# Performance work log

Measured on AMD Instinct MI355X. Metric: run time of the kernel, lower is better.

The kernel has to match this reference:

```python
import jax, jax.numpy as jnp
import numpy as np

T = 464
H = 256  # 256 * network_scale**2 with network_scale=1


def setup_inputs() -> dict:
    key = jax.random.key(0)
    ks = jax.random.split(key, 8)
    B = 64
    feature_encoded = jax.random.normal(ks[0], (B, T, H), dtype=jnp.float32)
    memory_state = jax.random.normal(ks[1], (B, H), dtype=jnp.float32) * 0.1
    carry_state = jax.random.normal(ks[2], (B, H), dtype=jnp.float32) * 0.1
    # LSTM params: kernel [H, 4H], recurrent kernel [H, 4H], bias [4H]; gate order i,f,c,o (Keras)
    # small init scale keeps the relu-activated recurrence numerically stable over 464 steps
    W = jax.random.normal(ks[3], (H, 4 * H), dtype=jnp.float32) * 0.02
    U = jax.random.normal(ks[4], (H, 4 * H), dtype=jnp.float32) * 0.02
    b = jnp.zeros((4 * H,), dtype=jnp.float32)
    # trailing dense: Flatten([B, T, H]) -> Dense(H, relu)
    Wd = jax.random.normal(ks[5], (T * H, H), dtype=jnp.float32) * (1.0 / np.sqrt(T * H))
    bd = jnp.zeros((H,), dtype=jnp.float32)
    return {"feature_encoded": feature_encoded, "memory_state": memory_state,
            "carry_state": carry_state, "W": W, "U": U, "b": b, "Wd": Wd, "bd": bd}


def _lstm_relu(x, h0, c0, W, U, b):
    # Keras LSTM with activation='relu', recurrent_activation='sigmoid'.
    def step(carry, x_t):
        h, c = carry
        z = x_t @ W + h @ U + b           # [B, 4H]
        zi, zf, zg, zo = jnp.split(z, 4, axis=-1)
        i = jax.nn.sigmoid(zi)
        f = jax.nn.sigmoid(zf)
        c = f * c + i * jax.nn.relu(zg)
        o = jax.nn.sigmoid(zo)
        h = o * jax.nn.relu(c)
        return (h, c), h

    xs = jnp.swapaxes(x, 0, 1)            # [T, B, H]
    (hT, cT), ys = jax.lax.scan(step, (h0, c0), xs)
    return jnp.swapaxes(ys, 0, 1), hT, cT  # [B, T, H], [B, H], [B, H]


def reference(feature_encoded, memory_state, carry_state, W, U, b, Wd, bd):
    B = feature_encoded.shape[0]
    x = feature_encoded.reshape(B, T, H)
    seq, hT, cT = _lstm_relu(x, memory_state, carry_state, W, U, b)
    flat = seq.reshape(B, T * H)
    core_output = jax.nn.relu(flat @ Wd + bd)  # [B, H]
    return core_output, hT, cT
```

## Files before the change

### kernel.cpp

```cpp
#include <hip/hip_runtime.h>

#define TT  464
#define HH  256
#define BB  64
#define NWG 64

using bf16x8 = __attribute__((ext_vector_type(8))) short;
using f32x4  = __attribute__((ext_vector_type(4))) float;

__device__ __forceinline__ unsigned short f2bf(float x) {
  union { float f; unsigned u; } v; v.f = x;
  unsigned r = v.u + 0x7fffu + ((v.u >> 16) & 1u);
  return (unsigned short)(r >> 16);
}

__device__ __forceinline__ void wait_flags(int* flags, int base, int target) {
  const int ln  = threadIdx.x & 63;
  int* p = &flags[base + (ln & 31)];
  for (;;) {
    int f = __hip_atomic_load(p, __ATOMIC_RELAXED, __HIP_MEMORY_SCOPE_AGENT);
    if (__all(f >= target)) break;
    __builtin_amdgcn_s_sleep(1);
  }
  asm volatile("" ::: "memory");
}

__global__ __launch_bounds__(256) void lstm_kernel(
    const float* __restrict__ x,
    const float* __restrict__ h0,
    const float* __restrict__ c0,
    const float* __restrict__ W,
    const float* __restrict__ U,
    const float* __restrict__ bias,
    unsigned int* __restrict__ h_bufs,
    unsigned short* __restrict__ seq,
    float* __restrict__ out,
    int* __restrict__ flags)
{
  const int tid = threadIdx.x;
  const int wg  = blockIdx.x;
  const int bgi = wg >> 5;
  const int fgi = wg & 31;
  const int wv  = tid >> 6;
  const int ln  = tid & 63;
  const int mt  = wv >> 1;
  const int nt  = wv & 1;
  const int l15 = ln & 15;
  const int q   = ln >> 4;

  __shared__ unsigned short Bt[32][520];
  __shared__ unsigned short x_lds[32][264];
  __shared__ float          z_lds[32][36];

  for (int it = 0; it < 64; ++it) {
    int i  = it * 256 + tid;
    int k  = i >> 5;
    int n  = i & 31;
    int gc = (n >> 3) * 256 + fgi * 8 + (n & 7);
    float wval = (k < 256) ? W[(size_t)k * 1024 + gc] : U[(size_t)(k - 256) * 1024 + gc];
    Bt[n][k] = f2bf(wval);
  }

  const int r_own = tid >> 3;
  const int j_own = tid & 7;
  const int brow  = bgi * 32 + r_own;
  const int col   = fgi * 8 + j_own;
  float c = c0[brow * HH + col];
  float h = h0[brow * HH + col];
  const float b_i = bias[        col];
  const float b_f = bias[  HH  + col];
  const float b_g = bias[2*HH  + col];
  const float b_o = bias[3*HH  + col];

  {
    unsigned short hb16 = f2bf(h);
    unsigned other = (unsigned)(unsigned short)__shfl_xor((int)hb16, 1);
    if (!(tid & 1)) {
      unsigned hpk = (unsigned)hb16 | (other << 16);
      __hip_atomic_store(&h_bufs[brow * 128 + (col >> 1)], hpk,
                         __ATOMIC_RELAXED, __HIP_MEMORY_SCOPE_AGENT);
    }
  }

  const int xc0  = j_own * 32;
  float4 xr[8];
  {
    const float4* p = (const float4*)(x + ((size_t)brow * TT + 0) * HH + xc0);
#pragma unroll
    for (int i = 0; i < 8; ++i) xr[i] = p[i];
  }

  __builtin_amdgcn_s_waitcnt(0);
  __syncthreads();
  if (tid == 0)
    __hip_atomic_store(&flags[wg], 1, __ATOMIC_RELAXED, __HIP_MEMORY_SCOPE_AGENT);

  for (int t = 0; t < TT; ++t) {
    const int pr  = t & 1;
    const int pwb = pr ^ 1;

    {
      unsigned px[16];
#pragma unroll
      for (int i = 0; i < 8; ++i) {
        px[2*i]   = (unsigned)f2bf(xr[i].x) | ((unsigned)f2bf(xr[i].y) << 16);
        px[2*i+1] = (unsigned)f2bf(xr[i].z) | ((unsigned)f2bf(xr[i].w) << 16);
      }
#pragma unroll
      for (int s = 0; s < 4; ++s) {
        uint4 v = make_uint4(px[4*s], px[4*s+1], px[4*s+2], px[4*s+3]);
        *(uint4*)&x_lds[r_own][xc0 + s * 8] = v;
      }
    }
    {
      const int tn = (t + 1 < TT) ? (t + 1) : (TT - 1);
      const float4* p = (const float4*)(x + ((size_t)brow * TT + tn) * HH + xc0);
#pragma unroll
      for (int i = 0; i < 8; ++i) xr[i] = p[i];
    }

    __syncthreads();

    f32x4 acc = {0.f, 0.f, 0.f, 0.f};
#pragma unroll
    for (int kk = 0; kk < 8; ++kk) {
      bf16x8 afr = *(const bf16x8*)&x_lds[mt * 16 + l15][kk * 32 + q * 8];
      bf16x8 bfr = *(const bf16x8*)&Bt[nt * 16 + l15][kk * 32 + q * 8];
      acc = __builtin_amdgcn_mfma_f32_16x16x32_bf16(afr, bfr, acc, 0, 0, 0);
    }

    wait_flags(flags, bgi * 32, t + 1);

    bf16x8 hf[8];
    {
      const unsigned long long* hb = (const unsigned long long*)h_bufs
          + (size_t)pr * (BB * HH / 4) + (bgi * 32 + mt * 16 + l15) * (HH / 4) + q * 2;
#pragma unroll
      for (int kk = 0; kk < 8; ++kk) {
        union { unsigned long long u[2]; bf16x8 v; } tmp;
        tmp.u[0] = __hip_atomic_load(hb + kk * 8 + 0, __ATOMIC_RELAXED, __HIP_MEMORY_SCOPE_AGENT);
        tmp.u[1] = __hip_atomic_load(hb + kk * 8 + 1, __ATOMIC_RELAXED, __HIP_MEMORY_SCOPE_AGENT);
        hf[kk] = tmp.v;
      }
    }
#pragma unroll
    for (int kk = 0; kk < 8; ++kk) {
      bf16x8 bfr = *(const bf16x8*)&Bt[nt * 16 + l15][256 + kk * 32 + q * 8];
      acc = __builtin_amdgcn_mfma_f32_16x16x32_bf16(hf[kk], bfr, acc, 0, 0, 0);
    }
#pragma unroll
    for (int reg = 0; reg < 4; ++reg)
      z_lds[mt * 16 + q * 4 + reg][nt * 16 + l15] = acc[reg];

    __syncthreads();

    float zi = z_lds[r_own][      j_own] + b_i;
    float zf = z_lds[r_own][ 8 + j_own] + b_f;
    float zg = z_lds[r_own][16 + j_own] + b_g;
    float zo = z_lds[r_own][24 + j_own] + b_o;
    float gi = 1.f / (1.f + __expf(-zi));
    float gf = 1.f / (1.f + __expf(-zf));
    float go = 1.f / (1.f + __expf(-zo));
    float gg = fmaxf(zg, 0.f);
    c = gf * c + gi * gg;
    h = go * fmaxf(c, 0.f);
    unsigned short hb16 = f2bf(h);
    seq[((size_t)brow * TT + t) * HH + col] = hb16;

    {
      unsigned other = (unsigned)(unsigned short)__shfl_xor((int)hb16, 1);
      if (!(tid & 1)) {
        unsigned hpk = (unsigned)hb16 | (other << 16);
        __hip_atomic_store(&h_bufs[pwb * (BB * 128) + brow * 128 + (col >> 1)], hpk,
                           __ATOMIC_RELAXED, __HIP_MEMORY_SCOPE_AGENT);
      }
    }
    __builtin_amdgcn_s_waitcnt(0);
    __syncthreads();
    if (tid == 0)
      __hip_atomic_store(&flags[wg], t + 2, __ATOMIC_RELAXED, __HIP_MEMORY_SCOPE_AGENT);
  }

  out[16384 + brow * HH + col] = h;
  out[32768 + brow * HH + col] = c;
}

#define DP_PA 264
#define DP_PW 258
__global__ __launch_bounds__(256) void dense_partial(
    const unsigned short* __restrict__ seq,
    const float* __restrict__ Wd,
    float* __restrict__ part)
{
  __shared__ __align__(16) char smem[64 * DP_PA * 2];
  unsigned short* a_lds = (unsigned short*)smem;
  float*          Wf    = (float*)smem;

  const int kb  = blockIdx.x;
  const int tid = threadIdx.x;
  const int wv  = tid >> 6;
  const int ln  = tid & 63;
  const int l15 = ln & 15;
  const int q   = ln >> 4;

  f32x4 acc[16];
#pragma unroll
  for (int i = 0; i < 16; ++i) acc[i] = (f32x4){0.f, 0.f, 0.f, 0.f};

  for (int half = 0; half < 2; ++half) {
    const int t = kb + half * 232;
    __syncthreads();
#pragma unroll
    for (int it = 0; it < 8; ++it) {
      int cidx = it * 256 + tid;
      int row  = cidx >> 5;
      int off  = (cidx & 31) * 8;
      *(bf16x8*)&a_lds[row * DP_PA + off] =
          *(const bf16x8*)(seq + ((size_t)row * TT + t) * HH + off);
    }
    __syncthreads();
    bf16x8 af[8];
#pragma unroll
    for (int kk = 0; kk < 8; ++kk)
      af[kk] = *(const bf16x8*)&a_lds[(wv * 16 + l15) * DP_PA + kk * 32 + q * 8];

    for (int ck = 0; ck < 8; ++ck) {
      __syncthreads();
#pragma unroll
      for (int it = 0; it < 8; ++it) {
        int idx = it * 256 + tid;
        int r   = idx >> 6;
        int c4  = (idx & 63) * 4;
        float4 v = *(const float4*)(Wd + ((size_t)(t * 256 + ck * 32 + r)) * HH + c4);
        *(float2*)&Wf[r * DP_PW + c4]     = make_float2(v.x, v.y);
        *(float2*)&Wf[r * DP_PW + c4 + 2] = make_float2(v.z, v.w);
      }
      __syncthreads();
#pragma unroll
      for (int nt2 = 0; nt2 < 16; ++nt2) {
        const int n = nt2 * 16 + l15;
        bf16x8 bfr;
#pragma unroll
        for (int j = 0; j < 8; ++j)
          bfr[j] = (short)f2bf(Wf[(q * 8 + j) * DP_PW + n]);
        acc[nt2] = __builtin_amdgcn_mfma_f32_16x16x32_bf16(af[ck], bfr, acc[nt2], 0, 0, 0);
      }
    }
  }

  float* pb = part + (size_t)kb * (BB * HH);
#pragma unroll
  for (int nt2 = 0; nt2 < 16; ++nt2)
#pragma unroll
    for (int reg = 0; reg < 4; ++reg)
      pb[(wv * 16 + q * 4 + reg) * HH + nt2 * 16 + l15] = acc[nt2][reg];
}

__global__ __launch_bounds__(256) void dense_reduce(
    const float* __restrict__ part,
    const float* __restrict__ bd,
    float* __restrict__ out)
{
  const int o = blockIdx.x * 256 + threadIdx.x;
  float s0 = 0.f, s1 = 0.f, s2 = 0.f, s3 = 0.f;
  for (int kb = 0; kb < 232; kb += 4) {
    s0 += part[(size_t)(kb    ) * 16384 + o];
    s1 += part[(size_t)(kb + 1) * 16384 + o];
    s2 += part[(size_t)(kb + 2) * 16384 + o];
    s3 += part[(size_t)(kb + 3) * 16384 + o];
  }
  float s = (s0 + s1) + (s2 + s3) + bd[o & 255];
  out[o] = fmaxf(s, 0.f);
}

extern "C" void kernel_launch(void* const* d_in, const int* in_sizes, int n_in,
                              void* d_out, int out_size, void* d_ws, size_t ws_size,
                              hipStream_t stream) {
  const float* x  = (const float*)d_in[0];
  const float* h0 = (const float*)d_in[1];
  const float* c0 = (const float*)d_in[2];
  const float* W  = (const float*)d_in[3];
  const float* U  = (const float*)d_in[4];
  const float* bv = (const float*)d_in[5];
  const float* Wd = (const float*)d_in[6];
  const float* bd = (const float*)d_in[7];
  float* out = (float*)d_out;

  char* w = (char*)d_ws;
  int* flags = (int*)w;
  unsigned int*   h_bufs = (unsigned int*)(w + 256);
  unsigned short* seq    = (unsigned short*)(w + 256 + 2 * BB * HH * 2);
  float*          part   = (float*)(w + 256 + 2 * BB * HH * 2 + (size_t)BB * TT * HH * 2);

  hipMemsetAsync(d_ws, 0, 256, stream);
  lstm_kernel<<<NWG, 256, 0, stream>>>(x, h0, c0, W, U, bv, h_bufs, seq, out, flags);
  dense_partial<<<232, 256, 0, stream>>>(seq, Wd, part);
  dense_reduce<<<64, 256, 0, stream>>>(part, bd, out);
}
```

Before: 2.334 ms.

## Replace flag barrier with step-tagged h values and keep LSTM weights in registers

```diff
diff --git a/kernel.cpp b/kernel.cpp
--- a/kernel.cpp
+++ b/kernel.cpp
@@ -7,6 +7,8 @@
 
 using bf16x8 = __attribute__((ext_vector_type(8))) short;
 using f32x4  = __attribute__((ext_vector_type(4))) float;
+typedef unsigned long long u64;
+typedef unsigned int u32;
 
 __device__ __forceinline__ unsigned short f2bf(float x) {
   union { float f; unsigned u; } v; v.f = x;
@@ -14,28 +16,16 @@
   return (unsigned short)(r >> 16);
 }
 
-__device__ __forceinline__ void wait_flags(int* flags, int base, int target) {
-  const int ln  = threadIdx.x & 63;
-  int* p = &flags[base + (ln & 31)];
-  for (;;) {
-    int f = __hip_atomic_load(p, __ATOMIC_RELAXED, __HIP_MEMORY_SCOPE_AGENT);
-    if (__all(f >= target)) break;
-    __builtin_amdgcn_s_sleep(1);
-  }
-  asm volatile("" ::: "memory");
-}
-
-__global__ __launch_bounds__(256) void lstm_kernel(
+__global__ __launch_bounds__(256, 1) void lstm_kernel(
     const float* __restrict__ x,
     const float* __restrict__ h0,
     const float* __restrict__ c0,
     const float* __restrict__ W,
     const float* __restrict__ U,
     const float* __restrict__ bias,
-    unsigned int* __restrict__ h_bufs,
+    u32* __restrict__ h_bufs,
     unsigned short* __restrict__ seq,
-    float* __restrict__ out,
-    int* __restrict__ flags)
+    float* __restrict__ out)
 {
   const int tid = threadIdx.x;
   const int wg  = blockIdx.x;
@@ -48,17 +38,19 @@
   const int l15 = ln & 15;
   const int q   = ln >> 4;
 
-  __shared__ unsigned short Bt[32][520];
-  __shared__ unsigned short x_lds[32][264];
-  __shared__ float          z_lds[32][36];
-
-  for (int it = 0; it < 64; ++it) {
-    int i  = it * 256 + tid;
-    int k  = i >> 5;
-    int n  = i & 31;
-    int gc = (n >> 3) * 256 + fgi * 8 + (n & 7);
-    float wval = (k < 256) ? W[(size_t)k * 1024 + gc] : U[(size_t)(k - 256) * 1024 + gc];
-    Bt[n][k] = f2bf(wval);
+  __shared__ float z_lds[2][32][36];
+
+  const int n  = nt * 16 + l15;
+  const int gc = (n >> 3) * 256 + fgi * 8 + (n & 7);
+  bf16x8 Bw[8], Bu[8];
+#pragma unroll
+  for (int kk = 0; kk < 8; ++kk) {
+#pragma unroll
+    for (int j = 0; j < 8; ++j) {
+      const int k = kk * 32 + q * 8 + j;
+      Bw[kk][j] = (short)f2bf(W[(size_t)k * 1024 + gc]);
+      Bu[kk][j] = (short)f2bf(U[(size_t)k * 1024 + gc]);
+    }
   }
 
   const int r_own = tid >> 3;
@@ -72,113 +64,98 @@
   const float b_g = bias[2*HH  + col];
   const float b_o = bias[3*HH  + col];
 
-  {
-    unsigned short hb16 = f2bf(h);
-    unsigned other = (unsigned)(unsigned short)__shfl_xor((int)hb16, 1);
-    if (!(tid & 1)) {
-      unsigned hpk = (unsigned)hb16 | (other << 16);
-      __hip_atomic_store(&h_bufs[brow * 128 + (col >> 1)], hpk,
-                         __ATOMIC_RELAXED, __HIP_MEMORY_SCOPE_AGENT);
-    }
-  }
-
-  const int xc0  = j_own * 32;
-  float4 xr[8];
-  {
-    const float4* p = (const float4*)(x + ((size_t)brow * TT + 0) * HH + xc0);
-#pragma unroll
-    for (int i = 0; i < 8; ++i) xr[i] = p[i];
-  }
-
-  __builtin_amdgcn_s_waitcnt(0);
-  __syncthreads();
-  if (tid == 0)
-    __hip_atomic_store(&flags[wg], 1, __ATOMIC_RELAXED, __HIP_MEMORY_SCOPE_AGENT);
+  __hip_atomic_store(&h_bufs[brow * HH + col],
+                     (1u << 16) | (u32)f2bf(h),
+                     __ATOMIC_RELAXED, __HIP_MEMORY_SCOPE_AGENT);
+
+  const int arow = bgi * 32 + mt * 16 + l15;
+  const float* xbase = x + (size_t)arow * TT * HH + q * 8;
+  float4 xf[16];
+#pragma unroll
+  for (int kk = 0; kk < 8; ++kk) {
+    xf[2*kk]   = *(const float4*)(xbase + kk * 32);
+    xf[2*kk+1] = *(const float4*)(xbase + kk * 32 + 4);
+  }
+
+  const u64* hrow0 = (const u64*)(h_bufs + arow * HH + q * 8);
+  const u64* hrow1 = (const u64*)(h_bufs + BB * HH + arow * HH + q * 8);
 
   for (int t = 0; t < TT; ++t) {
-    const int pr  = t & 1;
-    const int pwb = pr ^ 1;
-
-    {
-      unsigned px[16];
-#pragma unroll
-      for (int i = 0; i < 8; ++i) {
-        px[2*i]   = (unsigned)f2bf(xr[i].x) | ((unsigned)f2bf(xr[i].y) << 16);
-        px[2*i+1] = (unsigned)f2bf(xr[i].z) | ((unsigned)f2bf(xr[i].w) << 16);
+    const int pr = t & 1;
+
+    bf16x8 xa[8];
+#pragma unroll
+    for (int kk = 0; kk < 8; ++kk) {
+      union { u32 u[4]; bf16x8 v; } tmp;
+      tmp.u[0] = (u32)f2bf(xf[2*kk].x)   | ((u32)f2bf(xf[2*kk].y)   << 16);
+      tmp.u[1] = (u32)f2bf(xf[2*kk].z)   | ((u32)f2bf(xf[2*kk].w)   << 16);
+      tmp.u[2] = (u32)f2bf(xf[2*kk+1].x) | ((u32)f2bf(xf[2*kk+1].y) << 16);
+      tmp.u[3] = (u32)f2bf(xf[2*kk+1].z) | ((u32)f2bf(xf[2*kk+1].w) << 16);
+      xa[kk] = tmp.v;
+    }
+
+    f32x4 acc = {0.f, 0.f, 0.f, 0.f};
+#pragma unroll
+    for (int kk = 0; kk < 8; ++kk)
+      acc = __builtin_amdgcn_mfma_f32_16x16x32_bf16(xa[kk], Bw[kk], acc, 0, 0, 0);
+
+    const u64* hp = pr ? hrow1 : hrow0;
+    const u64 expd = ((u64)(u32)(t + 1) << 48) | ((u64)(u32)(t + 1) << 16);
+    u64 hv[32];
+    for (;;) {
+      u64 orv = 0;
+#pragma unroll
+      for (int kk = 0; kk < 8; ++kk)
+#pragma unroll
+        for (int pair = 0; pair < 4; ++pair) {
+          u64 v = __hip_atomic_load(hp + kk * 16 + pair,
+                                    __ATOMIC_RELAXED, __HIP_MEMORY_SCOPE_AGENT);
+          hv[kk * 4 + pair] = v;
+          orv |= v ^ expd;
+        }
+      if (__all((orv & 0xFFFF0000FFFF0000ull) == 0)) break;
+    }
+
+#pragma unroll
+    for (int kk = 0; kk < 8; ++kk) {
+      union { u32 u[4]; bf16x8 v; } tmp;
+#pragma unroll
+      for (int pair = 0; pair < 4; ++pair) {
+        u64 v = hv[kk * 4 + pair];
+        tmp.u[pair] = ((u32)v & 0xFFFFu) | ((u32)(v >> 32) << 16);
       }
-#pragma unroll
-      for (int s = 0; s < 4; ++s) {
-        uint4 v = make_uint4(px[4*s], px[4*s+1], px[4*s+2], px[4*s+3]);
-        *(uint4*)&x_lds[r_own][xc0 + s * 8] = v;
-      }
-    }
-    {
-      const int tn = (t + 1 < TT) ? (t + 1) : (TT - 1);
-      const float4* p = (const float4*)(x + ((size_t)brow * TT + tn) * HH + xc0);
-#pragma unroll
-      for (int i = 0; i < 8; ++i) xr[i] = p[i];
-    }
+      acc = __builtin_amdgcn_mfma_f32_16x16x32_bf16(tmp.v, Bu[kk], acc, 0, 0, 0);
+    }
+
+#pragma unroll
+    for (int reg = 0; reg < 4; ++reg)
+      z_lds[pr][mt * 16 + q * 4 + reg][nt * 16 + l15] = acc[reg];
 
     __syncthreads();
 
-    f32x4 acc = {0.f, 0.f, 0.f, 0.f};
-#pragma unroll
-    for (int kk = 0; kk < 8; ++kk) {
-      bf16x8 afr = *(const bf16x8*)&x_lds[mt * 16 + l15][kk * 32 + q * 8];
-      bf16x8 bfr = *(const bf16x8*)&Bt[nt * 16 + l15][kk * 32 + q * 8];
-      acc = __builtin_amdgcn_mfma_f32_16x16x32_bf16(afr, bfr, acc, 0, 0, 0);
-    }
-
-    wait_flags(flags, bgi * 32, t + 1);
-
-    bf16x8 hf[8];
-    {
-      const unsigned long long* hb = (const unsigned long long*)h_bufs
-          + (size_t)pr * (BB * HH / 4) + (bgi * 32 + mt * 16 + l15) * (HH / 4) + q * 2;
-#pragma unroll
-      for (int kk = 0; kk < 8; ++kk) {
-        union { unsigned long long u[2]; bf16x8 v; } tmp;
-        tmp.u[0] = __hip_atomic_load(hb + kk * 8 + 0, __ATOMIC_RELAXED, __HIP_MEMORY_SCOPE_AGENT);
-        tmp.u[1] = __hip_atomic_load(hb + kk * 8 + 1, __ATOMIC_RELAXED, __HIP_MEMORY_SCOPE_AGENT);
-        hf[kk] = tmp.v;
-      }
-    }
-#pragma unroll
-    for (int kk = 0; kk < 8; ++kk) {
-      bf16x8 bfr = *(const bf16x8*)&Bt[nt * 16 + l15][256 + kk * 32 + q * 8];
-      acc = __builtin_amdgcn_mfma_f32_16x16x32_bf16(hf[kk], bfr, acc, 0, 0, 0);
-    }
-#pragma unroll
-    for (int reg = 0; reg < 4; ++reg)
-      z_lds[mt * 16 + q * 4 + reg][nt * 16 + l15] = acc[reg];
-
-    __syncthreads();
-
-    float zi = z_lds[r_own][      j_own] + b_i;
-    float zf = z_lds[r_own][ 8 + j_own] + b_f;
-    float zg = z_lds[r_own][16 + j_own] + b_g;
-    float zo = z_lds[r_own][24 + j_own] + b_o;
+    float zi = z_lds[pr][r_own][      j_own] + b_i;
+    float zf = z_lds[pr][r_own][ 8 + j_own] + b_f;
+    float zg = z_lds[pr][r_own][16 + j_own] + b_g;
+    float zo = z_lds[pr][r_own][24 + j_own] + b_o;
     float gi = 1.f / (1.f + __expf(-zi));
     float gf = 1.f / (1.f + __expf(-zf));
     float go = 1.f / (1.f + __expf(-zo));
     float gg = fmaxf(zg, 0.f);
     c = gf * c + gi * gg;
     h = go * fmaxf(c, 0.f);
-    unsigned short hb16 = f2bf(h);
+    const unsigned short hb16 = f2bf(h);
     seq[((size_t)brow * TT + t) * HH + col] = hb16;
 
-    {
-      unsigned other = (unsigned)(unsigned short)__shfl_xor((int)hb16, 1);
-      if (!(tid & 1)) {
-        unsigned hpk = (unsigned)hb16 | (other << 16);
-        __hip_atomic_store(&h_bufs[pwb * (BB * 128) + brow * 128 + (col >> 1)], hpk,
-                           __ATOMIC_RELAXED, __HIP_MEMORY_SCOPE_AGENT);
-      }
-    }
-    __builtin_amdgcn_s_waitcnt(0);
-    __syncthreads();
-    if (tid == 0)
-      __hip_atomic_store(&flags[wg], t + 2, __ATOMIC_RELAXED, __HIP_MEMORY_SCOPE_AGENT);
+    __hip_atomic_store(&h_bufs[((t + 1) & 1) * (BB * HH) + brow * HH + col],
+                       ((u32)(t + 2) << 16) | (u32)hb16,
+                       __ATOMIC_RELAXED, __HIP_MEMORY_SCOPE_AGENT);
+
+    const int tn = (t + 1 < TT) ? (t + 1) : (TT - 1);
+#pragma unroll
+    for (int kk = 0; kk < 8; ++kk) {
+      xf[2*kk]   = *(const float4*)(xbase + (size_t)tn * HH + kk * 32);
+      xf[2*kk+1] = *(const float4*)(xbase + (size_t)tn * HH + kk * 32 + 4);
+    }
   }
 
   out[16384 + brow * HH + col] = h;
@@ -238,11 +215,11 @@
       __syncthreads();
 #pragma unroll
       for (int nt2 = 0; nt2 < 16; ++nt2) {
-        const int n = nt2 * 16 + l15;
+        const int nn = nt2 * 16 + l15;
         bf16x8 bfr;
 #pragma unroll
         for (int j = 0; j < 8; ++j)
-          bfr[j] = (short)f2bf(Wf[(q * 8 + j) * DP_PW + n]);
+          bfr[j] = (short)f2bf(Wf[(q * 8 + j) * DP_PW + nn]);
         acc[nt2] = __builtin_amdgcn_mfma_f32_16x16x32_bf16(af[ck], bfr, acc[nt2], 0, 0, 0);
       }
     }
@@ -287,13 +264,12 @@
   float* out = (float*)d_out;
 
   char* w = (char*)d_ws;
-  int* flags = (int*)w;
-  unsigned int*   h_bufs = (unsigned int*)(w + 256);
-  unsigned short* seq    = (unsigned short*)(w + 256 + 2 * BB * HH * 2);
-  float*          part   = (float*)(w + 256 + 2 * BB * HH * 2 + (size_t)BB * TT * HH * 2);
-
-  hipMemsetAsync(d_ws, 0, 256, stream);
-  lstm_kernel<<<NWG, 256, 0, stream>>>(x, h0, c0, W, U, bv, h_bufs, seq, out, flags);
+  u32*            h_bufs = (u32*)w;
+  unsigned short* seq    = (unsigned short*)(w + 2 * BB * HH * 4);
+  float*          part   = (float*)(w + 2 * BB * HH * 4 + (size_t)BB * TT * HH * 2);
+
+  hipMemsetAsync(h_bufs, 0, 2 * BB * HH * 4, stream);
+  lstm_kernel<<<NWG, 256, 0, stream>>>(x, h0, c0, W, U, bv, h_bufs, seq, out);
   dense_partial<<<232, 256, 0, stream>>>(seq, Wd, part);
   dense_reduce<<<64, 256, 0, stream>>>(part, bd, out);
 }
```

Result: slower. 3.359 ms (+43.9%).
